# Kernel tuning notes

Hardware: AMD Instinct MI355X
Metric: run time of the kernel (lower is better)

## Reference

```python
import jax, jax.numpy as jnp
import numpy as np

B, N, X, H = 128, 512, 128, 256  # batch, seq len, in features, hidden

_PARAM_SHAPES = [
    ("fg_w_c", (H,)), ("fg_w_h", (H, H)), ("fg_w_x", (H, X)), ("fg_b", (H,)),
    ("ig_w_c", (H,)), ("ig_w_h", (H, H)), ("ig_w_x", (H, X)), ("ig_b", (H,)),
    ("in_w_h", (H, H)), ("in_w_x", (H, X)), ("in_b", (H,)),
    ("og_w_cn", (H,)), ("og_w_h", (H, H)), ("og_w_x", (H, X)), ("og_b", (H,)), ("og_w_t", (H,)),
    ("tg1_w_x", (H, X)), ("tg1_w_t", (H,)), ("tg1_b", (H,)),
    ("tg2_w_x", (H, X)), ("tg2_w_t", (H,)), ("tg2_b", (H,)),
]


def setup_inputs() -> dict:
    key = jax.random.key(0)
    ks = jax.random.split(key, 2 + len(_PARAM_SHAPES))
    stdv = 1.0 / np.sqrt(H)  # torch __init__ re-inits all params uniform(-stdv, stdv)
    inp = {
        "x": jax.random.normal(ks[0], (B, N, X), jnp.float32),
        "t": jax.random.uniform(ks[1], (B, N, 1), jnp.float32),  # time intervals >= 0
    }
    for i, (name, shape) in enumerate(_PARAM_SHAPES):
        inp[name] = jax.random.uniform(ks[2 + i], shape, jnp.float32, -stdv, stdv)
    return inp


def reference(x, t,
              fg_w_c, fg_w_h, fg_w_x, fg_b,
              ig_w_c, ig_w_h, ig_w_x, ig_b,
              in_w_h, in_w_x, in_b,
              og_w_cn, og_w_h, og_w_x, og_b, og_w_t,
              tg1_w_x, tg1_w_t, tg1_b,
              tg2_w_x, tg2_w_t, tg2_b):
    # TimeLSTM_v3 with nn_type = NN_TYPE_LSTM_TIME2.
    # torch stores vector params as [H,1] and x_cur as [B,xm,1]; here squeezed to [H] / [B,xm].
    # Precompute all input-dependent (non-recurrent) gate terms over the whole sequence: [B,N,H]
    fg_x = jnp.einsum('bnx,hx->bnh', x, fg_w_x) + fg_b
    ig_x = jnp.einsum('bnx,hx->bnh', x, ig_w_x) + ig_b
    in_x = jnp.einsum('bnx,hx->bnh', x, in_w_x) + in_b
    og_x = jnp.einsum('bnx,hx->bnh', x, og_w_x) + og_w_t * t + og_b
    # Time gates depend only on x and t -> fully precomputable
    tm1 = jax.nn.sigmoid(jnp.einsum('bnx,hx->bnh', x, tg1_w_x) + jnp.tanh(tg1_w_t * t) + tg1_b)
    tm2 = jax.nn.sigmoid(jnp.einsum('bnx,hx->bnh', x, tg2_w_x) + jnp.tanh(tg2_w_t * t) + tg2_b)

    def step(carry, inputs):
        h, cm = carry  # each [B,H]
        fg_xt, ig_xt, in_xt, og_xt, tm1_t, tm2_t = inputs
        ig = jax.nn.sigmoid(ig_w_c * cm + h @ ig_w_h.T + ig_xt)
        fg = jax.nn.sigmoid(fg_w_c * cm + h @ fg_w_h.T + fg_xt)
        inn = jnp.tanh(h @ in_w_h.T + in_xt)
        cm_hat = fg * cm + ig * tm1_t * inn
        cm_new = fg * cm + ig * tm2_t * inn
        og = jax.nn.sigmoid(og_w_cn * cm_hat + h @ og_w_h.T + og_xt)
        h_new = og * jnp.tanh(cm_hat)
        return (h_new, cm_new), None

    seqs = tuple(jnp.moveaxis(a, 1, 0) for a in (fg_x, ig_x, in_x, og_x, tm1, tm2))  # [N,B,H]
    init = (jnp.zeros((x.shape[0], H), x.dtype), jnp.zeros((x.shape[0], H), x.dtype))
    (h, cm), _ = jax.lax.scan(step, init, seqs)
    return h, cm  # h: [B,H] (torch squeezes trailing 1), cm: [B,H]
```

## Files before the change

kernel.cpp:

```cpp
#include <hip/hip_runtime.h>
#include <math.h>

#define BATCH 128
#define SEQN  512
#define XF    128
#define HF    256
#define BC    16
#define HC    8
#define TCH   8
#define NBLK  256
#define NTHR  256
#define NGRP  8
#define GSZ   32
#define NS    20

#define OFF_WX   0
#define OFF_G    6144
#define OFF_XS   12288
#define OFF_H    28672
#define OFF_CM   32768
#define OFF_COEF 32896
#define OFF_GO   32992
#define LDS_WORDS 32996
#define LDS_BYTES (LDS_WORDS * 4)

struct Params {
  const float* x;
  const float* t;
  const float* w_h[4];
  const float* w_x[6];
  const float* coef[12];
  float* h_buf;
  unsigned* flags;
  float* out;
};

__device__ __forceinline__ float sigmoidf_(float v) { return 1.0f / (1.0f + __expf(-v)); }
__device__ __forceinline__ float tanhf_(float x) {
  const float e = __expf(2.0f * x);
  return 1.0f - 2.0f / (e + 1.0f);
}

__device__ __forceinline__ float swzx1(float v) { return __int_as_float(__builtin_amdgcn_ds_swizzle(__float_as_int(v), 0x041F)); }
__device__ __forceinline__ float swzx2(float v) { return __int_as_float(__builtin_amdgcn_ds_swizzle(__float_as_int(v), 0x081F)); }
__device__ __forceinline__ float swzx4(float v) { return __int_as_float(__builtin_amdgcn_ds_swizzle(__float_as_int(v), 0x101F)); }
__device__ __forceinline__ float swzx8(float v) { return __int_as_float(__builtin_amdgcn_ds_swizzle(__float_as_int(v), 0x201F)); }

__device__ __forceinline__ void post_arrive(unsigned* flags, int gi, int mi, unsigned val) {
  __syncthreads();
  if (threadIdx.x == 0) {
    __hip_atomic_store(&flags[(gi * GSZ + mi) * 16], val,
                       __ATOMIC_RELAXED, __HIP_MEMORY_SCOPE_AGENT);
  }
}

__global__ __launch_bounds__(NTHR, 1) void timelstm_kernel(Params p) {
  extern __shared__ float sm[];
  const int tid = threadIdx.x;
  const int bid = blockIdx.x;
  const int gi = bid & 7;
  const int mi = bid >> 3;
  const int b0 = gi * BC;
  const int h0 = mi * HC;

  const int lane = tid & 63;
  const int bq = tid >> 6;
  const int kh = lane & 7;
  const int j  = lane >> 3;

  float wrs[4][32];
#pragma unroll
  for (int g = 0; g < 4; ++g)
#pragma unroll
    for (int q = 0; q < 8; ++q) {
      const float4 v = *(const float4*)&p.w_h[g][(size_t)(h0 + j) * HF + kh * 32 + q * 4];
      wrs[g][q * 4 + 0] = v.x; wrs[g][q * 4 + 1] = v.y;
      wrs[g][q * 4 + 2] = v.z; wrs[g][q * 4 + 3] = v.w;
    }
  for (int i = tid; i < 6 * 8 * 128; i += NTHR) {
    int g = i >> 10, jj = (i >> 7) & 7, k = i & 127;
    sm[OFF_WX + k * 48 + jj * 6 + g] = p.w_x[g][(h0 + jj) * XF + k];
  }
  if (tid < 96) sm[OFF_COEF + tid] = p.coef[tid >> 3][h0 + (tid & 7)];
  if (tid < 128) sm[OFF_CM + tid] = 0.0f;
  if (tid == 0) *(unsigned*)&sm[OFF_GO] = 0u;
  if (mi == 0) {
    unsigned long long* hbu = (unsigned long long*)p.h_buf + (size_t)b0 * (HF / 2);
    for (int i = tid; i < BC * HF / 2; i += NTHR) {
      __hip_atomic_store(&hbu[i], 0ull, __ATOMIC_RELAXED, __HIP_MEMORY_SCOPE_AGENT);
    }
  }
  post_arrive(p.flags, gi, mi, 1u);

  float a0[4], a1[4], a2[4], a3[4], a4[4], a5[4];
  float tvr[4];
#pragma unroll
  for (int u = 0; u < 4; ++u) { a0[u]=0.f; a1[u]=0.f; a2[u]=0.f; a3[u]=0.f; a4[u]=0.f; a5[u]=0.f; }
  int tc_next = 0;
  int sc = 0;
  const int cc = tid >> 3, rr = tid & 7;
  const int c4 = cc << 2;

  auto do_slice = [&](int s) {
    if (s < 4) {
      if (s == 0) {
#pragma unroll
        for (int u = 0; u < 4; ++u) {
          const int bt = c4 + u;
          tvr[u] = p.t[(size_t)(b0 + (bt >> 3)) * SEQN + tc_next + (bt & 7)];
        }
      }
      float4 xr[4];
#pragma unroll
      for (int q = 0; q < 4; ++q) {
        const int it = s * 4 + q;
        const int bt = (bq << 5) + it * 2 + (lane >> 5);
        xr[q] = *(const float4*)&p.x[((size_t)(b0 + (bt >> 3)) * SEQN + (tc_next + (bt & 7))) * XF + (lane & 31) * 4];
      }
#pragma unroll
      for (int q = 0; q < 4; ++q) {
        const int it = s * 4 + q;
        const int bt = (bq << 5) + it * 2 + (lane >> 5);
        const int k0 = (lane & 31) * 4;
        const float xb[4] = {xr[q].x, xr[q].y, xr[q].z, xr[q].w};
#pragma unroll
        for (int u = 0; u < 4; ++u) {
          const int k = k0 + u;
          sm[OFF_XS + k * 128 + (bt ^ (((k >> 2) & 7) << 2))] = xb[u];
        }
      }
    } else {
      const float* wxp = &sm[OFF_WX + rr * 6];
      const int kbase = (s - 4) * 8;
#pragma unroll
      for (int kk = 0; kk < 8; ++kk) {
        const int k = kbase + kk;
        const float4 xv = *(const float4*)&sm[OFF_XS + k * 128 + (c4 ^ (((k >> 2) & 7) << 2))];
        const float2 wA = *(const float2*)&wxp[k * 48 + 0];
        const float2 wB = *(const float2*)&wxp[k * 48 + 2];
        const float2 wC = *(const float2*)&wxp[k * 48 + 4];
        const float xs[4] = {xv.x, xv.y, xv.z, xv.w};
#pragma unroll
        for (int u = 0; u < 4; ++u) {
          a0[u] += wA.x * xs[u]; a1[u] += wA.y * xs[u];
          a2[u] += wB.x * xs[u]; a3[u] += wB.y * xs[u];
          a4[u] += wC.x * xs[u]; a5[u] += wC.y * xs[u];
        }
      }
    }
  };

  auto dump_G = [&]() {
    const float cfg  = sm[OFF_COEF + 0 * 8 + rr], cig  = sm[OFF_COEF + 1 * 8 + rr];
    const float cin  = sm[OFF_COEF + 2 * 8 + rr];
    const float cogb = sm[OFF_COEF + 3 * 8 + rr], cogwt = sm[OFF_COEF + 4 * 8 + rr];
    const float ct1w = sm[OFF_COEF + 5 * 8 + rr], ct1b = sm[OFF_COEF + 6 * 8 + rr];
    const float ct2w = sm[OFF_COEF + 7 * 8 + rr], ct2b = sm[OFF_COEF + 8 * 8 + rr];
#pragma unroll
    for (int u = 0; u < 4; ++u) {
      const int bt = c4 + u, b = bt >> 3, t = bt & 7;
      const float tv = tvr[u];
      float* gp = &sm[OFF_G + t * 768 + b * 8 + rr];
      gp[0]   = a0[u] + cfg;
      gp[128] = a1[u] + cig;
      gp[256] = a2[u] + cin;
      gp[384] = a3[u] + cogwt * tv + cogb;
      gp[512] = sigmoidf_(a4[u] + tanhf_(ct1w * tv) + ct1b);
      gp[640] = sigmoidf_(a5[u] + tanhf_(ct2w * tv) + ct2b);
      a0[u] = 0.f; a1[u] = 0.f; a2[u] = 0.f; a3[u] = 0.f; a4[u] = 0.f; a5[u] = 0.f;
    }
  };

  auto wave_wait_s = [&](unsigned target) {
    unsigned* go = (unsigned*)&sm[OFF_GO];
    if (tid < 64) {
      const bool need = tid < GSZ;
      const unsigned* f = &p.flags[(gi * GSZ + (tid & (GSZ - 1))) * 16];
      while (true) {
        unsigned v = need ? __hip_atomic_load(f, __ATOMIC_RELAXED, __HIP_MEMORY_SCOPE_AGENT)
                          : target;
        if (__all((int)(v >= target))) break;
        if (sc < NS) { do_slice(sc); ++sc; }
      }
      if (tid == 0)
        __hip_atomic_store(go, target, __ATOMIC_RELAXED, __HIP_MEMORY_SCOPE_WORKGROUP);
    } else {
      while (true) {
        unsigned v = __hip_atomic_load(go, __ATOMIC_RELAXED, __HIP_MEMORY_SCOPE_WORKGROUP);
        if (v >= target) break;
        if (sc < NS) { do_slice(sc); ++sc; }
      }
    }
    asm volatile("" ::: "memory");
  };

  for (int s = 0; s < NS; ++s) do_slice(s);
  dump_G();

  unsigned tstep = 1;
  int cur = 0;

  for (int tc0 = 0; tc0 < SEQN; tc0 += TCH) {
    tc_next = tc0 + TCH;
    sc = (tc_next < SEQN) ? 0 : NS;

    for (int tt = 0; tt < TCH; ++tt) {
      wave_wait_s(tstep);
      {
        const unsigned long long* hsrc = (const unsigned long long*)
            (p.h_buf + (size_t)cur * BATCH * HF + (size_t)(b0 + (bq << 2)) * HF);
        unsigned long long v[4][2];
#pragma unroll
        for (int u = 0; u < 4; ++u) {
          const unsigned long long* src = hsrc + (size_t)u * (HF / 2) + lane * 2;
          v[u][0] = __hip_atomic_load(src,     __ATOMIC_RELAXED, __HIP_MEMORY_SCOPE_AGENT);
          v[u][1] = __hip_atomic_load(src + 1, __ATOMIC_RELAXED, __HIP_MEMORY_SCOPE_AGENT);
        }
        float f[4][4];
#pragma unroll
        for (int u = 0; u < 4; ++u) {
          union { unsigned long long u64; float2 f2; } x0, x1;
          x0.u64 = v[u][0]; x1.u64 = v[u][1];
          f[u][0] = x0.f2.x; f[u][1] = x0.f2.y; f[u][2] = x1.f2.x; f[u][3] = x1.f2.y;
        }
        const int swz = ((lane >> 3) & 7) << 2;
        const int wbase = OFF_H + (bq << 10);
#pragma unroll
        for (int e = 0; e < 4; ++e) {
          const int a = wbase + (((lane << 4) + (e << 2)) ^ swz);
          float2 lo = {f[0][e], f[1][e]};
          float2 hi = {f[2][e], f[3][e]};
          *(float2*)&sm[a]     = lo;
          *(float2*)&sm[a + 2] = hi;
        }
      }

      float acc[4][4];
#pragma unroll
      for (int bi = 0; bi < 4; ++bi)
#pragma unroll
        for (int g = 0; g < 4; ++g) acc[bi][g] = 0.f;

      const int hbase = OFF_H + (bq << 10) + (kh << 7);
      const int khx = kh << 2;
#pragma unroll
      for (int kk = 0; kk < 32; ++kk) {
        const int off = ((((kk & 7) << 2) ^ khx)) + ((kk >> 3) << 5);
        const float4 hv = *(const float4*)&sm[hbase + off];
        const float w0 = wrs[0][kk], w1 = wrs[1][kk], w2 = wrs[2][kk], w3 = wrs[3][kk];
        acc[0][0] += hv.x * w0; acc[0][1] += hv.x * w1; acc[0][2] += hv.x * w2; acc[0][3] += hv.x * w3;
        acc[1][0] += hv.y * w0; acc[1][1] += hv.y * w1; acc[1][2] += hv.y * w2; acc[1][3] += hv.y * w3;
        acc[2][0] += hv.z * w0; acc[2][1] += hv.z * w1; acc[2][2] += hv.z * w2; acc[2][3] += hv.z * w3;
        acc[3][0] += hv.w * w0; acc[3][1] += hv.w * w1; acc[3][2] += hv.w * w2; acc[3][3] += hv.w * w3;
      }

      const int kb0 = kh & 1, kb1 = (kh >> 1) & 1;
      float s1[2][4];
#pragma unroll
      for (int pp = 0; pp < 2; ++pp)
#pragma unroll
        for (int g = 0; g < 4; ++g) {
          const float mine  = kb0 ? acc[2 * pp + 1][g] : acc[2 * pp][g];
          const float yours = kb0 ? acc[2 * pp][g]     : acc[2 * pp + 1][g];
          s1[pp][g] = mine + swzx1(yours);
        }
      float s2[4];
#pragma unroll
      for (int g = 0; g < 4; ++g) {
        const float mine  = kb1 ? s1[1][g] : s1[0][g];
        const float yours = kb1 ? s1[0][g] : s1[1][g];
        s2[g] = mine + swzx2(yours);
      }
      float pre[4];
#pragma unroll
      for (int g = 0; g < 4; ++g) pre[g] = s2[g] + swzx4(s2[g]);

      {
        const int bi = kh & 3;
        const int b  = (bq << 2) + bi;
        const int ib = b * 8 + j;
        const float cm = sm[OFF_CM + ib];
        const float* gt = &sm[OFF_G + tt * 768 + ib];
        const float fgx = gt[0],   igx = gt[128], inx = gt[256];
        const float ogx = gt[384], tm1 = gt[512], tm2 = gt[640];
        const float igv = sigmoidf_(sm[OFF_COEF + 10 * 8 + j] * cm + pre[1] + igx);
        const float fgv = sigmoidf_(sm[OFF_COEF + 9 * 8 + j] * cm + pre[0] + fgx);
        const float inn = tanhf_(pre[2] + inx);
        const float cbase = fgv * cm, cinn = igv * inn;
        const float cmh = cbase + cinn * tm1;
        const float cmn = cbase + cinn * tm2;
        const float ogv = sigmoidf_(sm[OFF_COEF + 11 * 8 + j] * cmh + pre[3] + ogx);
        const float hn  = ogv * tanhf_(cmh);
        const float hn2 = swzx8(hn);
        if (kh < 4) {
          sm[OFF_CM + ib] = cmn;
          if (!(j & 1)) {
            union { float2 f; unsigned long long u; } cv;
            cv.f.x = hn; cv.f.y = hn2;
            unsigned long long* hdst =
                (unsigned long long*)(p.h_buf + (size_t)(cur ^ 1) * BATCH * HF +
                                      (size_t)(b0 + b) * HF + h0 + j);
            __hip_atomic_store(hdst, cv.u, __ATOMIC_RELAXED, __HIP_MEMORY_SCOPE_AGENT);
          }
          if (tc0 + tt == SEQN - 1) {
            p.out[(size_t)(b0 + b) * HF + h0 + j] = hn;
            p.out[(size_t)BATCH * HF + (size_t)(b0 + b) * HF + h0 + j] = cmn;
          }
        }
      }
      post_arrive(p.flags, gi, mi, tstep + 1);
      ++tstep;
      cur ^= 1;
    }

    if (tc_next < SEQN) {
      while (sc < NS) { do_slice(sc); ++sc; }
      dump_G();
    }
  }
}

extern "C" void kernel_launch(void* const* d_in, const int* in_sizes, int n_in,
                              void* d_out, int out_size, void* d_ws, size_t ws_size,
                              hipStream_t stream) {
  (void)in_sizes; (void)n_in; (void)out_size; (void)ws_size;
  Params p;
  p.x = (const float*)d_in[0];
  p.t = (const float*)d_in[1];
  p.w_h[0] = (const float*)d_in[3];
  p.w_h[1] = (const float*)d_in[7];
  p.w_h[2] = (const float*)d_in[10];
  p.w_h[3] = (const float*)d_in[14];
  p.w_x[0] = (const float*)d_in[4];
  p.w_x[1] = (const float*)d_in[8];
  p.w_x[2] = (const float*)d_in[11];
  p.w_x[3] = (const float*)d_in[15];
  p.w_x[4] = (const float*)d_in[18];
  p.w_x[5] = (const float*)d_in[21];
  p.coef[0]  = (const float*)d_in[5];
  p.coef[1]  = (const float*)d_in[9];
  p.coef[2]  = (const float*)d_in[12];
  p.coef[3]  = (const float*)d_in[16];
  p.coef[4]  = (const float*)d_in[17];
  p.coef[5]  = (const float*)d_in[19];
  p.coef[6]  = (const float*)d_in[20];
  p.coef[7]  = (const float*)d_in[22];
  p.coef[8]  = (const float*)d_in[23];
  p.coef[9]  = (const float*)d_in[2];
  p.coef[10] = (const float*)d_in[6];
  p.coef[11] = (const float*)d_in[13];
  p.flags = (unsigned*)d_ws;
  p.h_buf = (float*)((char*)d_ws + 32768);
  p.out = (float*)d_out;

  (void)hipMemsetAsync(d_ws, 0, 16384, stream);
  (void)hipFuncSetAttribute((const void*)timelstm_kernel,
                            hipFuncAttributeMaxDynamicSharedMemorySize, LDS_BYTES);
  timelstm_kernel<<<dim3(NBLK), dim3(NTHR), LDS_BYTES, stream>>>(p);
}
```

Baseline: 2.874 ms.

## Replace flag barriers with step-tagged h values and inline per-chunk x projection

Removes the per-block arrival flags and the __syncthreads-based post/wait handshake. Each hidden value is now written as a 64-bit word that packs the step number with the float, and readers spin on the h words until every tag matches the expected step. The x-projection work that was interleaved into spin-wait slices is now computed in one go at the start of each 8-step chunk. This aims to cut the flag round-trip and barrier latency on the serial critical path. In exchange each h store doubles in size, the spin loop reloads all 16 words per retry, and the projection can no longer hide inside wait time.

```diff
diff --git a/kernel.cpp b/kernel.cpp
--- a/kernel.cpp
+++ b/kernel.cpp
@@ -12,7 +12,6 @@
 #define NTHR  256
 #define NGRP  8
 #define GSZ   32
-#define NS    20
 
 #define OFF_WX   0
 #define OFF_G    6144
@@ -20,8 +19,7 @@
 #define OFF_H    28672
 #define OFF_CM   32768
 #define OFF_COEF 32896
-#define OFF_GO   32992
-#define LDS_WORDS 32996
+#define LDS_WORDS 32992
 #define LDS_BYTES (LDS_WORDS * 4)
 
 struct Params {
@@ -30,8 +28,7 @@
   const float* w_h[4];
   const float* w_x[6];
   const float* coef[12];
-  float* h_buf;
-  unsigned* flags;
+  unsigned long long* h_tag;
   float* out;
 };
 
@@ -44,15 +41,7 @@
 __device__ __forceinline__ float swzx1(float v) { return __int_as_float(__builtin_amdgcn_ds_swizzle(__float_as_int(v), 0x041F)); }
 __device__ __forceinline__ float swzx2(float v) { return __int_as_float(__builtin_amdgcn_ds_swizzle(__float_as_int(v), 0x081F)); }
 __device__ __forceinline__ float swzx4(float v) { return __int_as_float(__builtin_amdgcn_ds_swizzle(__float_as_int(v), 0x101F)); }
-__device__ __forceinline__ float swzx8(float v) { return __int_as_float(__builtin_amdgcn_ds_swizzle(__float_as_int(v), 0x201F)); }
-
-__device__ __forceinline__ void post_arrive(unsigned* flags, int gi, int mi, unsigned val) {
-  __syncthreads();
-  if (threadIdx.x == 0) {
-    __hip_atomic_store(&flags[(gi * GSZ + mi) * 16], val,
-                       __ATOMIC_RELAXED, __HIP_MEMORY_SCOPE_AGENT);
-  }
-}
+
 
 __global__ __launch_bounds__(NTHR, 1) void timelstm_kernel(Params p) {
   extern __shared__ float sm[];
@@ -67,6 +56,8 @@
   const int bq = tid >> 6;
   const int kh = lane & 7;
   const int j  = lane >> 3;
+  const int cc = tid >> 3, rr = tid & 7;
+  const int c4 = cc << 2;
 
   float wrs[4][32];
 #pragma unroll
@@ -83,58 +74,48 @@
   }
   if (tid < 96) sm[OFF_COEF + tid] = p.coef[tid >> 3][h0 + (tid & 7)];
   if (tid < 128) sm[OFF_CM + tid] = 0.0f;
-  if (tid == 0) *(unsigned*)&sm[OFF_GO] = 0u;
-  if (mi == 0) {
-    unsigned long long* hbu = (unsigned long long*)p.h_buf + (size_t)b0 * (HF / 2);
-    for (int i = tid; i < BC * HF / 2; i += NTHR) {
-      __hip_atomic_store(&hbu[i], 0ull, __ATOMIC_RELAXED, __HIP_MEMORY_SCOPE_AGENT);
-    }
-  }
-  post_arrive(p.flags, gi, mi, 1u);
-
-  float a0[4], a1[4], a2[4], a3[4], a4[4], a5[4];
-  float tvr[4];
-#pragma unroll
-  for (int u = 0; u < 4; ++u) { a0[u]=0.f; a1[u]=0.f; a2[u]=0.f; a3[u]=0.f; a4[u]=0.f; a5[u]=0.f; }
-  int tc_next = 0;
-  int sc = 0;
-  const int cc = tid >> 3, rr = tid & 7;
-  const int c4 = cc << 2;
-
-  auto do_slice = [&](int s) {
-    if (s < 4) {
-      if (s == 0) {
-#pragma unroll
-        for (int u = 0; u < 4; ++u) {
-          const int bt = c4 + u;
-          tvr[u] = p.t[(size_t)(b0 + (bt >> 3)) * SEQN + tc_next + (bt & 7)];
-        }
-      }
-      float4 xr[4];
-#pragma unroll
-      for (int q = 0; q < 4; ++q) {
-        const int it = s * 4 + q;
-        const int bt = (bq << 5) + it * 2 + (lane >> 5);
-        xr[q] = *(const float4*)&p.x[((size_t)(b0 + (bt >> 3)) * SEQN + (tc_next + (bt & 7))) * XF + (lane & 31) * 4];
-      }
-#pragma unroll
-      for (int q = 0; q < 4; ++q) {
-        const int it = s * 4 + q;
-        const int bt = (bq << 5) + it * 2 + (lane >> 5);
-        const int k0 = (lane & 31) * 4;
-        const float xb[4] = {xr[q].x, xr[q].y, xr[q].z, xr[q].w};
-#pragma unroll
-        for (int u = 0; u < 4; ++u) {
-          const int k = k0 + u;
-          sm[OFF_XS + k * 128 + (bt ^ (((k >> 2) & 7) << 2))] = xb[u];
-        }
-      }
-    } else {
+  __syncthreads();
+
+  unsigned tstep = 1;
+
+  for (int tc0 = 0; tc0 < SEQN; tc0 += TCH) {
+    {
+#pragma unroll
+      for (int half = 0; half < 2; ++half) {
+        float4 xr[8];
+#pragma unroll
+        for (int q = 0; q < 8; ++q) {
+          const int it = half * 8 + q;
+          const int bt = (bq << 5) + it * 2 + (lane >> 5);
+          xr[q] = *(const float4*)&p.x[((size_t)(b0 + (bt >> 3)) * SEQN + (tc0 + (bt & 7))) * XF + (lane & 31) * 4];
+        }
+#pragma unroll
+        for (int q = 0; q < 8; ++q) {
+          const int it = half * 8 + q;
+          const int bt = (bq << 5) + it * 2 + (lane >> 5);
+          const int k0 = (lane & 31) * 4;
+          const float xb[4] = {xr[q].x, xr[q].y, xr[q].z, xr[q].w};
+#pragma unroll
+          for (int u = 0; u < 4; ++u) {
+            const int k = k0 + u;
+            sm[OFF_XS + k * 128 + (bt ^ (((k >> 2) & 7) << 2))] = xb[u];
+          }
+        }
+      }
+    }
+    {
+      float tvr[4];
+#pragma unroll
+      for (int u = 0; u < 4; ++u) {
+        const int bt = c4 + u;
+        tvr[u] = p.t[(size_t)(b0 + (bt >> 3)) * SEQN + tc0 + (bt & 7)];
+      }
+      float a0[4], a1[4], a2[4], a3[4], a4[4], a5[4];
+#pragma unroll
+      for (int u = 0; u < 4; ++u) { a0[u]=0.f; a1[u]=0.f; a2[u]=0.f; a3[u]=0.f; a4[u]=0.f; a5[u]=0.f; }
       const float* wxp = &sm[OFF_WX + rr * 6];
-      const int kbase = (s - 4) * 8;
-#pragma unroll
-      for (int kk = 0; kk < 8; ++kk) {
-        const int k = kbase + kk;
+#pragma unroll 4
+      for (int k = 0; k < XF; ++k) {
         const float4 xv = *(const float4*)&sm[OFF_XS + k * 128 + (c4 ^ (((k >> 2) & 7) << 2))];
         const float2 wA = *(const float2*)&wxp[k * 48 + 0];
         const float2 wB = *(const float2*)&wxp[k * 48 + 2];
@@ -147,92 +128,53 @@
           a4[u] += wC.x * xs[u]; a5[u] += wC.y * xs[u];
         }
       }
-    }
-  };
-
-  auto dump_G = [&]() {
-    const float cfg  = sm[OFF_COEF + 0 * 8 + rr], cig  = sm[OFF_COEF + 1 * 8 + rr];
-    const float cin  = sm[OFF_COEF + 2 * 8 + rr];
-    const float cogb = sm[OFF_COEF + 3 * 8 + rr], cogwt = sm[OFF_COEF + 4 * 8 + rr];
-    const float ct1w = sm[OFF_COEF + 5 * 8 + rr], ct1b = sm[OFF_COEF + 6 * 8 + rr];
-    const float ct2w = sm[OFF_COEF + 7 * 8 + rr], ct2b = sm[OFF_COEF + 8 * 8 + rr];
-#pragma unroll
-    for (int u = 0; u < 4; ++u) {
-      const int bt = c4 + u, b = bt >> 3, t = bt & 7;
-      const float tv = tvr[u];
-      float* gp = &sm[OFF_G + t * 768 + b * 8 + rr];
-      gp[0]   = a0[u] + cfg;
-      gp[128] = a1[u] + cig;
-      gp[256] = a2[u] + cin;
-      gp[384] = a3[u] + cogwt * tv + cogb;
-      gp[512] = sigmoidf_(a4[u] + tanhf_(ct1w * tv) + ct1b);
-      gp[640] = sigmoidf_(a5[u] + tanhf_(ct2w * tv) + ct2b);
-      a0[u] = 0.f; a1[u] = 0.f; a2[u] = 0.f; a3[u] = 0.f; a4[u] = 0.f; a5[u] = 0.f;
-    }
-  };
-
-  auto wave_wait_s = [&](unsigned target) {
-    unsigned* go = (unsigned*)&sm[OFF_GO];
-    if (tid < 64) {
-      const bool need = tid < GSZ;
-      const unsigned* f = &p.flags[(gi * GSZ + (tid & (GSZ - 1))) * 16];
+      const float cfg  = sm[OFF_COEF + 0 * 8 + rr], cig  = sm[OFF_COEF + 1 * 8 + rr];
+      const float cin  = sm[OFF_COEF + 2 * 8 + rr];
+      const float cogb = sm[OFF_COEF + 3 * 8 + rr], cogwt = sm[OFF_COEF + 4 * 8 + rr];
+      const float ct1w = sm[OFF_COEF + 5 * 8 + rr], ct1b = sm[OFF_COEF + 6 * 8 + rr];
+      const float ct2w = sm[OFF_COEF + 7 * 8 + rr], ct2b = sm[OFF_COEF + 8 * 8 + rr];
+#pragma unroll
+      for (int u = 0; u < 4; ++u) {
+        const int bt = c4 + u, b = bt >> 3, t = bt & 7;
+        const float tv = tvr[u];
+        float* gp = &sm[OFF_G + t * 768 + b * 8 + rr];
+        gp[0]   = a0[u] + cfg;
+        gp[128] = a1[u] + cig;
+        gp[256] = a2[u] + cin;
+        gp[384] = a3[u] + cogwt * tv + cogb;
+        gp[512] = sigmoidf_(a4[u] + tanhf_(ct1w * tv) + ct1b);
+        gp[640] = sigmoidf_(a5[u] + tanhf_(ct2w * tv) + ct2b);
+      }
+    }
+
+    for (int tt = 0; tt < TCH; ++tt) {
+      const unsigned target = tstep - 1;
+      const unsigned long long* hsrc =
+          p.h_tag + (size_t)((tstep - 1) & 1) * BATCH * HF +
+          (size_t)(b0 + (bq << 2)) * HF;
+      unsigned long long v[16];
       while (true) {
-        unsigned v = need ? __hip_atomic_load(f, __ATOMIC_RELAXED, __HIP_MEMORY_SCOPE_AGENT)
-                          : target;
-        if (__all((int)(v >= target))) break;
-        if (sc < NS) { do_slice(sc); ++sc; }
-      }
-      if (tid == 0)
-        __hip_atomic_store(go, target, __ATOMIC_RELAXED, __HIP_MEMORY_SCOPE_WORKGROUP);
-    } else {
-      while (true) {
-        unsigned v = __hip_atomic_load(go, __ATOMIC_RELAXED, __HIP_MEMORY_SCOPE_WORKGROUP);
-        if (v >= target) break;
-        if (sc < NS) { do_slice(sc); ++sc; }
-      }
-    }
-    asm volatile("" ::: "memory");
-  };
-
-  for (int s = 0; s < NS; ++s) do_slice(s);
-  dump_G();
-
-  unsigned tstep = 1;
-  int cur = 0;
-
-  for (int tc0 = 0; tc0 < SEQN; tc0 += TCH) {
-    tc_next = tc0 + TCH;
-    sc = (tc_next < SEQN) ? 0 : NS;
-
-    for (int tt = 0; tt < TCH; ++tt) {
-      wave_wait_s(tstep);
-      {
-        const unsigned long long* hsrc = (const unsigned long long*)
-            (p.h_buf + (size_t)cur * BATCH * HF + (size_t)(b0 + (bq << 2)) * HF);
-        unsigned long long v[4][2];
-#pragma unroll
-        for (int u = 0; u < 4; ++u) {
-          const unsigned long long* src = hsrc + (size_t)u * (HF / 2) + lane * 2;
-          v[u][0] = __hip_atomic_load(src,     __ATOMIC_RELAXED, __HIP_MEMORY_SCOPE_AGENT);
-          v[u][1] = __hip_atomic_load(src + 1, __ATOMIC_RELAXED, __HIP_MEMORY_SCOPE_AGENT);
-        }
-        float f[4][4];
-#pragma unroll
-        for (int u = 0; u < 4; ++u) {
-          union { unsigned long long u64; float2 f2; } x0, x1;
-          x0.u64 = v[u][0]; x1.u64 = v[u][1];
-          f[u][0] = x0.f2.x; f[u][1] = x0.f2.y; f[u][2] = x1.f2.x; f[u][3] = x1.f2.y;
-        }
-        const int swz = ((lane >> 3) & 7) << 2;
-        const int wbase = OFF_H + (bq << 10);
-#pragma unroll
-        for (int e = 0; e < 4; ++e) {
-          const int a = wbase + (((lane << 4) + (e << 2)) ^ swz);
-          float2 lo = {f[0][e], f[1][e]};
-          float2 hi = {f[2][e], f[3][e]};
-          *(float2*)&sm[a]     = lo;
-          *(float2*)&sm[a + 2] = hi;
-        }
+#pragma unroll
+        for (int u = 0; u < 4; ++u)
+#pragma unroll
+          for (int q = 0; q < 4; ++q)
+            v[u * 4 + q] = __hip_atomic_load(&hsrc[(size_t)u * HF + q * 64 + lane],
+                                             __ATOMIC_RELAXED, __HIP_MEMORY_SCOPE_AGENT);
+        bool ok = true;
+#pragma unroll
+        for (int i = 0; i < 16; ++i) ok &= ((unsigned)(v[i] >> 32) == target);
+        if (__all((int)ok)) break;
+      }
+#pragma unroll
+      for (int q = 0; q < 4; ++q) {
+        const int k = q * 64 + lane;
+        float4 w;
+        w.x = __uint_as_float((unsigned)v[0 * 4 + q]);
+        w.y = __uint_as_float((unsigned)v[1 * 4 + q]);
+        w.z = __uint_as_float((unsigned)v[2 * 4 + q]);
+        w.w = __uint_as_float((unsigned)v[3 * 4 + q]);
+        const int a = OFF_H + (bq << 10) + ((k * 4) ^ (((k >> 5) & 7) << 2));
+        *(float4*)&sm[a] = w;
       }
 
       float acc[4][4];
@@ -291,31 +233,20 @@
         const float cmn = cbase + cinn * tm2;
         const float ogv = sigmoidf_(sm[OFF_COEF + 11 * 8 + j] * cmh + pre[3] + ogx);
         const float hn  = ogv * tanhf_(cmh);
-        const float hn2 = swzx8(hn);
         if (kh < 4) {
           sm[OFF_CM + ib] = cmn;
-          if (!(j & 1)) {
-            union { float2 f; unsigned long long u; } cv;
-            cv.f.x = hn; cv.f.y = hn2;
-            unsigned long long* hdst =
-                (unsigned long long*)(p.h_buf + (size_t)(cur ^ 1) * BATCH * HF +
-                                      (size_t)(b0 + b) * HF + h0 + j);
-            __hip_atomic_store(hdst, cv.u, __ATOMIC_RELAXED, __HIP_MEMORY_SCOPE_AGENT);
-          }
+          const unsigned long long pv =
+              ((unsigned long long)tstep << 32) | (unsigned long long)__float_as_uint(hn);
+          __hip_atomic_store(&p.h_tag[(size_t)(tstep & 1) * BATCH * HF +
+                                      (size_t)(b0 + b) * HF + h0 + j],
+                             pv, __ATOMIC_RELAXED, __HIP_MEMORY_SCOPE_AGENT);
           if (tc0 + tt == SEQN - 1) {
             p.out[(size_t)(b0 + b) * HF + h0 + j] = hn;
             p.out[(size_t)BATCH * HF + (size_t)(b0 + b) * HF + h0 + j] = cmn;
           }
         }
       }
-      post_arrive(p.flags, gi, mi, tstep + 1);
       ++tstep;
-      cur ^= 1;
-    }
-
-    if (tc_next < SEQN) {
-      while (sc < NS) { do_slice(sc); ++sc; }
-      dump_G();
     }
   }
 }
@@ -349,11 +280,10 @@
   p.coef[9]  = (const float*)d_in[2];
   p.coef[10] = (const float*)d_in[6];
   p.coef[11] = (const float*)d_in[13];
-  p.flags = (unsigned*)d_ws;
-  p.h_buf = (float*)((char*)d_ws + 32768);
+  p.h_tag = (unsigned long long*)d_ws;
   p.out = (float*)d_out;
 
-  (void)hipMemsetAsync(d_ws, 0, 16384, stream);
+  (void)hipMemsetAsync(d_ws, 0, (size_t)2 * BATCH * HF * 8, stream);
   (void)hipFuncSetAttribute((const void*)timelstm_kernel,
                             hipFuncAttributeMaxDynamicSharedMemorySize, LDS_BYTES);
   timelstm_kernel<<<dim3(NBLK), dim3(NTHR), LDS_BYTES, stream>>>(p);
```

Result: slower. 3.169 ms (+10.3%).
